# Kernel tuning notes

Measured on AMD Instinct MI355X. Metric: run time of the kernel, lower is better.

The kernel has to match this reference:

```python
import jax, jax.numpy as jnp
import numpy as np

B, S, F, H, C = 8, 512, 32, 256, 128

def _ln(x, g, b, eps=1e-5):
    m = jnp.mean(x, -1, keepdims=True)
    v = jnp.var(x, -1, keepdims=True)
    return (x - m) * jax.lax.rsqrt(v + eps) * g + b

def setup_inputs():
    key = jax.random.key(0)
    ks = jax.random.split(key, 16)
    def n(i, shape, s=0.05):
        return jax.random.normal(ks[i], shape, jnp.float32) * s
    d = {}
    d['x'] = jax.random.normal(ks[0], (B, S, F), jnp.float32)
    d['context'] = jax.random.normal(ks[1], (B, C), jnp.float32)
    # per-feature GRNs, params stacked over F (input_size=1 -> weight is [F,H])
    d['w1'] = n(2, (F, H)); d['b1'] = jnp.zeros((F, H), jnp.float32)
    d['w2'] = n(3, (F, H, H)); d['b2'] = jnp.zeros((F, H), jnp.float32)
    d['wg'] = n(4, (F, H, 2 * H)); d['bg'] = jnp.zeros((F, 2 * H), jnp.float32)
    d['ws'] = n(5, (F, H)); d['bs'] = jnp.zeros((F, H), jnp.float32)
    d['g1'] = jnp.ones((F, H), jnp.float32); d['be1'] = jnp.zeros((F, H), jnp.float32)
    # selection GRN: input F*H, hidden H, output F, context C
    d['sw1'] = n(6, (F * H, H)); d['sb1'] = jnp.zeros((H,), jnp.float32)
    d['sctx'] = n(7, (C, H))
    d['sw2'] = n(8, (H, H)); d['sb2'] = jnp.zeros((H,), jnp.float32)
    d['sgw'] = n(9, (H, 2 * F)); d['sgb'] = jnp.zeros((2 * F,), jnp.float32)
    d['sg'] = jnp.ones((F,), jnp.float32); d['sbt'] = jnp.zeros((F,), jnp.float32)
    d['skw'] = n(10, (F * H, F)); d['skb'] = jnp.zeros((F,), jnp.float32)
    # output GRN: H -> H, identity skip
    d['ow1'] = n(11, (H, H)); d['ob1'] = jnp.zeros((H,), jnp.float32)
    d['ow2'] = n(12, (H, H)); d['ob2'] = jnp.zeros((H,), jnp.float32)
    d['ogw'] = n(13, (H, 2 * H)); d['ogb'] = jnp.zeros((2 * H,), jnp.float32)
    d['og'] = jnp.ones((H,), jnp.float32); d['obt'] = jnp.zeros((H,), jnp.float32)
    return d

def _forward(x, context, w1, b1, w2, b2, wg, bg, ws, bs, g1, be1,
             sw1, sb1, sctx, sw2, sb2, sgw, sgb, sg, sbt, skw, skb,
             ow1, ob1, ow2, ob2, ogw, ogb, og, obt):
    elu = jax.nn.elu
    xe = x[..., None]                                   # [B,S,F,1]
    # --- per-feature GRNs, batched over F (dropout = identity in eval) ---
    h = elu(xe * w1 + b1)                               # [B,S,F,H]
    h = elu(jnp.einsum('bsfh,fhk->bsfk', h, w2) + b2)   # [B,S,F,H]
    gates = jnp.einsum('bsfh,fhk->bsfk', h, wg) + bg    # [B,S,F,2H]
    glu = gates[..., :H] * jax.nn.sigmoid(gates[..., H:])
    skip = xe * ws + bs                                 # skip_layer (1 -> H)
    stacked = _ln(glu + skip, g1, be1)                  # [B,S,F,H]
    # --- selection GRN on flattened features, with context enrichment ---
    flat = stacked.reshape(x.shape[0], x.shape[1], F * H)
    sskip = flat @ skw + skb                            # [B,S,F]
    hs = elu(flat @ sw1 + sb1)
    hs = hs + (context @ sctx)[:, None, :]              # expand ctx over seq
    hs = elu(hs @ sw2 + sb2)
    gg = hs @ sgw + sgb
    glu2 = gg[..., :F] * jax.nn.sigmoid(gg[..., F:])
    weights = jax.nn.softmax(_ln(glu2 + sskip, sg, sbt), axis=-1)  # [B,S,F]
    # --- softmax-weighted feature fusion ---
    combined = jnp.einsum('bsfh,bsf->bsh', stacked, weights)       # [B,S,H]
    # --- output GRN (identity skip) ---
    ho = elu(combined @ ow1 + ob1)
    ho = elu(ho @ ow2 + ob2)
    go = ho @ ogw + ogb
    glu3 = go[..., :H] * jax.nn.sigmoid(go[..., H:])
    out = _ln(glu3 + combined, og, obt)
    return out, weights

def reference(x, context, w1, b1, w2, b2, wg, bg, ws, bs, g1, be1,
              sw1, sb1, sctx, sw2, sb2, sgw, sgb, sg, sbt, skw, skb,
              ow1, ob1, ow2, ob2, ogw, ogb, og, obt):
    return _forward(x, context, w1, b1, w2, b2, wg, bg, ws, bs, g1, be1,
                    sw1, sb1, sctx, sw2, sb2, sgw, sgb, sg, sbt, skw, skb,
                    ow1, ob1, ow2, ob2, ogw, ogb, og, obt)
```

## Files before the change

### kernel.cpp

```cpp
#include <hip/hip_runtime.h>

#define TTOT 4096
#define FDIM 32
#define HDIM 256
#define CDIM 128

__device__ __forceinline__ float eluf(float z){ return z > 0.f ? z : __expf(z) - 1.f; }
__device__ __forceinline__ float sigf(float z){ return 1.f / (1.f + __expf(-z)); }

__device__ __forceinline__ void zero84(float a[8][4]){
#pragma unroll
  for (int t = 0; t < 8; ++t){ a[t][0] = a[t][1] = a[t][2] = a[t][3] = 0.f; }
}

__device__ __forceinline__ void gemm_8x4(const float* __restrict__ A, int lda,
                                         const float* __restrict__ W, int ldw,
                                         int tb, int K, float acc[8][4]){
  for (int h0 = 0; h0 < K; h0 += 8){
    float4 wr[8];
#pragma unroll
    for (int r = 0; r < 8; ++r) wr[r] = *(const float4*)(W + (h0 + r)*ldw);
#pragma unroll
    for (int t = 0; t < 8; ++t){
      const float* ap = A + (tb + t)*lda + h0;
      float4 a0 = *(const float4*)ap;
      float4 a1 = *(const float4*)(ap + 4);
      float av[8] = {a0.x, a0.y, a0.z, a0.w, a1.x, a1.y, a1.z, a1.w};
#pragma unroll
      for (int r = 0; r < 8; ++r){
        acc[t][0] = fmaf(av[r], wr[r].x, acc[t][0]);
        acc[t][1] = fmaf(av[r], wr[r].y, acc[t][1]);
        acc[t][2] = fmaf(av[r], wr[r].z, acc[t][2]);
        acc[t][3] = fmaf(av[r], wr[r].w, acc[t][3]);
      }
    }
  }
}

__device__ __forceinline__ void feature_grn(
    const int f, const int tid, const float* __restrict__ xsf,
    const float* __restrict__ w1, const float* __restrict__ b1,
    const float* __restrict__ w2, const float* __restrict__ b2,
    const float* __restrict__ wg, const float* __restrict__ bg,
    const float* __restrict__ wsk, const float* __restrict__ bsk,
    const float* __restrict__ g1, const float* __restrict__ be1,
    float* __restrict__ bufA, float* __restrict__ bufB,
    float* __restrict__ mS, float* __restrict__ rS)
{
  const int kg = tid & 63, tg = tid >> 6;
  const int k0 = kg*4, tb = tg*8;

  {
    const float w1v = w1[f*HDIM + tid];
    const float b1v = b1[f*HDIM + tid];
#pragma unroll 8
    for (int t = 0; t < 32; ++t) bufA[t*256 + tid] = eluf(xsf[t*8]*w1v + b1v);
  }
  __syncthreads();

  {
    float acc[8][4]; zero84(acc);
    gemm_8x4(bufA, 256, w2 + (size_t)f*65536 + k0, 256, tb, 256, acc);
    const float4 bv = *(const float4*)(b2 + f*HDIM + k0);
#pragma unroll
    for (int t = 0; t < 8; ++t){
      float4 o;
      o.x = eluf(acc[t][0] + bv.x); o.y = eluf(acc[t][1] + bv.y);
      o.z = eluf(acc[t][2] + bv.z); o.w = eluf(acc[t][3] + bv.w);
      *(float4*)(bufB + (tb + t)*256 + k0) = o;
    }
  }
  __syncthreads();

  {
    float accA[8][4], accB[8][4]; zero84(accA); zero84(accB);
    const float* wgf = wg + (size_t)f*131072;
    gemm_8x4(bufB, 256, wgf + k0,       512, tb, 256, accA);
    gemm_8x4(bufB, 256, wgf + 256 + k0, 512, tb, 256, accB);
    const float4 bga = *(const float4*)(bg + f*512 + k0);
    const float4 bgb = *(const float4*)(bg + f*512 + 256 + k0);
    const float4 wsv = *(const float4*)(wsk + f*HDIM + k0);
    const float4 bsv = *(const float4*)(bsk + f*HDIM + k0);
    const float ba[4] = {bga.x, bga.y, bga.z, bga.w};
    const float bb[4] = {bgb.x, bgb.y, bgb.z, bgb.w};
    const float wa[4] = {wsv.x, wsv.y, wsv.z, wsv.w};
    const float sa[4] = {bsv.x, bsv.y, bsv.z, bsv.w};
#pragma unroll
    for (int t = 0; t < 8; ++t){
      const float xv = xsf[(tb + t)*8];
      float o[4];
#pragma unroll
      for (int j = 0; j < 4; ++j){
        const float ga = accA[t][j] + ba[j];
        const float gb = accB[t][j] + bb[j];
        o[j] = ga*sigf(gb) + fmaf(xv, wa[j], sa[j]);
      }
      *(float4*)(bufA + (tb + t)*256 + k0) = make_float4(o[0], o[1], o[2], o[3]);
    }
  }
  __syncthreads();

  {
    const int tt = tid >> 3, j = tid & 7;
    float s = 0.f, s2 = 0.f;
#pragma unroll 8
    for (int i = 0; i < 32; ++i){
      const float v = bufA[tt*256 + j + i*8];
      s += v; s2 = fmaf(v, v, s2);
    }
    s += __shfl_xor(s, 1); s2 += __shfl_xor(s2, 1);
    s += __shfl_xor(s, 2); s2 += __shfl_xor(s2, 2);
    s += __shfl_xor(s, 4); s2 += __shfl_xor(s2, 4);
    if (j == 0){
      const float m = s * (1.f/256.f);
      mS[tt] = m;
      rS[tt] = rsqrtf(s2*(1.f/256.f) - m*m + 1e-5f);
    }
  }
  __syncthreads();

  {
    const float gv = g1[f*HDIM + tid];
    const float bv = be1[f*HDIM + tid];
#pragma unroll 4
    for (int t = 0; t < 32; ++t)
      bufB[t*256 + tid] = (bufA[t*256 + tid] - mS[t])*rS[t]*gv + bv;
  }
  __syncthreads();
}

template<int STORE>
__global__ __launch_bounds__(256, 2) void k_feat(
    const float* __restrict__ x,
    const float* __restrict__ w1, const float* __restrict__ b1,
    const float* __restrict__ w2, const float* __restrict__ b2,
    const float* __restrict__ wg, const float* __restrict__ bg,
    const float* __restrict__ wsk, const float* __restrict__ bsk,
    const float* __restrict__ g1, const float* __restrict__ be1,
    const float* __restrict__ sw1, const float* __restrict__ skw,
    float* __restrict__ z1_part, float* __restrict__ sskip_part,
    float* __restrict__ stacked)
{
  const int t0 = blockIdx.x * 32;
  const int fg = blockIdx.y;
  const int tid = threadIdx.x;
  __shared__ float xs8[32*8];
  __shared__ float mS[32], rS[32];
  __shared__ __align__(16) float bufA[8192];
  __shared__ __align__(16) float bufB[8192];

  {
    const int r = tid >> 3, c = tid & 7;
    xs8[r*8 + c] = x[(t0 + r)*FDIM + fg*8 + c];
  }
  const int kg = tid & 63, tg = tid >> 6;
  const int k0 = kg*4, tb = tg*8;
  const int tt = tid >> 3, j0 = (tid & 7)*4;

  float acc_sel[8][4]; zero84(acc_sel);
  float acc_skip[4] = {0.f, 0.f, 0.f, 0.f};
  __syncthreads();

  for (int i = 0; i < 8; ++i){
    const int f = fg*8 + i;
    feature_grn(f, tid, xs8 + i, w1, b1, w2, b2, wg, bg, wsk, bsk, g1, be1,
                bufA, bufB, mS, rS);
    gemm_8x4(bufB, 256, sw1 + (size_t)f*65536 + k0, 256, tb, 256, acc_sel);
    for (int h = 0; h < 256; h += 4){
      const float4 a = *(const float4*)(bufB + tt*256 + h);
      const size_t rb = ((size_t)f*256 + h)*32 + j0;
      const float4 s0 = *(const float4*)(skw + rb);
      const float4 s1 = *(const float4*)(skw + rb + 32);
      const float4 s2 = *(const float4*)(skw + rb + 64);
      const float4 s3 = *(const float4*)(skw + rb + 96);
      acc_skip[0] = fmaf(a.x, s0.x, fmaf(a.y, s1.x, fmaf(a.z, s2.x, fmaf(a.w, s3.x, acc_skip[0]))));
      acc_skip[1] = fmaf(a.x, s0.y, fmaf(a.y, s1.y, fmaf(a.z, s2.y, fmaf(a.w, s3.y, acc_skip[1]))));
      acc_skip[2] = fmaf(a.x, s0.z, fmaf(a.y, s1.z, fmaf(a.z, s2.z, fmaf(a.w, s3.z, acc_skip[2]))));
      acc_skip[3] = fmaf(a.x, s0.w, fmaf(a.y, s1.w, fmaf(a.z, s2.w, fmaf(a.w, s3.w, acc_skip[3]))));
    }
    if (STORE){
      float* outp = stacked + (size_t)t0*8192 + f*256 + tid;
#pragma unroll 4
      for (int t = 0; t < 32; ++t) outp[(size_t)t*8192] = bufB[t*256 + tid];
    }
  }

  float* zp = z1_part + (size_t)fg*TTOT*HDIM + (size_t)t0*256;
#pragma unroll
  for (int t = 0; t < 8; ++t)
    *(float4*)(zp + (tb + t)*256 + k0) =
        make_float4(acc_sel[t][0], acc_sel[t][1], acc_sel[t][2], acc_sel[t][3]);
  float* sp = sskip_part + (size_t)fg*TTOT*32 + (size_t)t0*32;
  *(float4*)(sp + tt*32 + j0) =
      make_float4(acc_skip[0], acc_skip[1], acc_skip[2], acc_skip[3]);
}

__global__ __launch_bounds__(256, 2) void k_feat2(
    const float* __restrict__ x,
    const float* __restrict__ w1, const float* __restrict__ b1,
    const float* __restrict__ w2, const float* __restrict__ b2,
    const float* __restrict__ wg, const float* __restrict__ bg,
    const float* __restrict__ wsk, const float* __restrict__ bsk,
    const float* __restrict__ g1, const float* __restrict__ be1,
    const float* __restrict__ wts,
    float* __restrict__ cmb_part)
{
  const int t0 = blockIdx.x * 32;
  const int fg = blockIdx.y;
  const int tid = threadIdx.x;
  __shared__ float xs8[32*8];
  __shared__ float wt8[32*8];
  __shared__ float mS[32], rS[32];
  __shared__ __align__(16) float bufA[8192];
  __shared__ __align__(16) float bufB[8192];

  {
    const int r = tid >> 3, c = tid & 7;
    xs8[r*8 + c] = x[(t0 + r)*FDIM + fg*8 + c];
    wt8[r*8 + c] = wts[(t0 + r)*FDIM + fg*8 + c];
  }
  const int kg = tid & 63, tg = tid >> 6;
  const int k0 = kg*4, tb = tg*8;
  float acc_cmb[8][4]; zero84(acc_cmb);
  __syncthreads();

  for (int i = 0; i < 8; ++i){
    const int f = fg*8 + i;
    feature_grn(f, tid, xs8 + i, w1, b1, w2, b2, wg, bg, wsk, bsk, g1, be1,
                bufA, bufB, mS, rS);
#pragma unroll
    for (int t = 0; t < 8; ++t){
      const float wv = wt8[(tb + t)*8 + i];
      const float4 a = *(const float4*)(bufB + (tb + t)*256 + k0);
      acc_cmb[t][0] = fmaf(wv, a.x, acc_cmb[t][0]);
      acc_cmb[t][1] = fmaf(wv, a.y, acc_cmb[t][1]);
      acc_cmb[t][2] = fmaf(wv, a.z, acc_cmb[t][2]);
      acc_cmb[t][3] = fmaf(wv, a.w, acc_cmb[t][3]);
    }
  }
  float* cp = cmb_part + (size_t)fg*TTOT*HDIM + (size_t)t0*256;
#pragma unroll
  for (int t = 0; t < 8; ++t)
    *(float4*)(cp + (tb + t)*256 + k0) =
        make_float4(acc_cmb[t][0], acc_cmb[t][1], acc_cmb[t][2], acc_cmb[t][3]);
}

__global__ __launch_bounds__(256) void k_sel2(
    const float* __restrict__ z1_part,
    const float* __restrict__ sb1,
    const float* __restrict__ context, const float* __restrict__ sctx,
    const float* __restrict__ sw2, const float* __restrict__ sb2,
    const float* __restrict__ sgw, const float* __restrict__ sgb,
    const float* __restrict__ sg, const float* __restrict__ sbt,
    const float* __restrict__ sskip_part, const float* __restrict__ skb,
    float* __restrict__ wout)
{
  const int t0 = blockIdx.x * 32;
  const int tid = threadIdx.x;
  __shared__ __align__(16) float A[8192];
  __shared__ __align__(16) float Bm[8192];
  __shared__ float ggs[32*64];
  __shared__ float pn[32*32];

  float cxv = 0.f;
  {
    const float* cb = context + (size_t)(t0 >> 9)*CDIM;
    for (int c = 0; c < CDIM; ++c) cxv = fmaf(cb[c], sctx[c*HDIM + tid], cxv);
  }
  {
    const float sbv = sb1[tid];
    const float* p0 = z1_part + (size_t)t0*256;
    const float* p1 = p0 + (size_t)TTOT*HDIM;
    const float* p2 = p0 + (size_t)2*TTOT*HDIM;
    const float* p3 = p0 + (size_t)3*TTOT*HDIM;
#pragma unroll 4
    for (int i = 0; i < 32; ++i){
      const int idx = i*256 + tid;
      A[idx] = eluf(p0[idx] + p1[idx] + p2[idx] + p3[idx] + sbv) + cxv;
    }
  }
  __syncthreads();
  const int kg = tid & 63, tg = tid >> 6;
  const int k0 = kg*4, tb = tg*8;
  {
    float acc[8][4]; zero84(acc);
    gemm_8x4(A, 256, sw2 + k0, 256, tb, 256, acc);
    const float4 bv = *(const float4*)(sb2 + k0);
#pragma unroll
    for (int t = 0; t < 8; ++t){
      float4 o;
      o.x = eluf(acc[t][0] + bv.x); o.y = eluf(acc[t][1] + bv.y);
      o.z = eluf(acc[t][2] + bv.z); o.w = eluf(acc[t][3] + bv.w);
      *(float4*)(Bm + (tb + t)*256 + k0) = o;
    }
  }
  __syncthreads();
  {
    const int t = tid >> 3, jg = tid & 7;
    float a8[8] = {0.f,0.f,0.f,0.f,0.f,0.f,0.f,0.f};
    for (int h = 0; h < 256; ++h){
      const float v = Bm[t*256 + h];
      const float4 wA = *(const float4*)(sgw + h*64 + jg*8);
      const float4 wB = *(const float4*)(sgw + h*64 + jg*8 + 4);
      a8[0] = fmaf(v, wA.x, a8[0]); a8[1] = fmaf(v, wA.y, a8[1]);
      a8[2] = fmaf(v, wA.z, a8[2]); a8[3] = fmaf(v, wA.w, a8[3]);
      a8[4] = fmaf(v, wB.x, a8[4]); a8[5] = fmaf(v, wB.y, a8[5]);
      a8[6] = fmaf(v, wB.z, a8[6]); a8[7] = fmaf(v, wB.w, a8[7]);
    }
#pragma unroll
    for (int j = 0; j < 8; ++j) ggs[t*64 + jg*8 + j] = a8[j] + sgb[jg*8 + j];
  }
  __syncthreads();
  for (int i = tid; i < 1024; i += 256){
    const int t = i >> 5, j = i & 31;
    const size_t si = (size_t)(t0 + t)*32 + j;
    const float ss = sskip_part[si] + sskip_part[si + (size_t)TTOT*32]
                   + sskip_part[si + (size_t)2*TTOT*32]
                   + sskip_part[si + (size_t)3*TTOT*32] + skb[j];
    pn[i] = ggs[t*64 + j]*sigf(ggs[t*64 + 32 + j]) + ss;
  }
  __syncthreads();
  {
    const int tt = tid >> 3, j = tid & 7;
    float v[4]; float s = 0.f, s2 = 0.f;
#pragma unroll
    for (int i = 0; i < 4; ++i){ v[i] = pn[tt*32 + j + i*8]; s += v[i]; s2 = fmaf(v[i], v[i], s2); }
    s += __shfl_xor(s, 1); s2 += __shfl_xor(s2, 1);
    s += __shfl_xor(s, 2); s2 += __shfl_xor(s2, 2);
    s += __shfl_xor(s, 4); s2 += __shfl_xor(s2, 4);
    const float m = s*(1.f/32.f);
    const float rstd = rsqrtf(s2*(1.f/32.f) - m*m + 1e-5f);
    float zv[4]; float mx = -1e30f;
#pragma unroll
    for (int i = 0; i < 4; ++i){
      const int fi = j + i*8;
      zv[i] = (v[i] - m)*rstd*sg[fi] + sbt[fi];
      mx = fmaxf(mx, zv[i]);
    }
    mx = fmaxf(mx, __shfl_xor(mx, 1));
    mx = fmaxf(mx, __shfl_xor(mx, 2));
    mx = fmaxf(mx, __shfl_xor(mx, 4));
    float e[4]; float se = 0.f;
#pragma unroll
    for (int i = 0; i < 4; ++i){ e[i] = __expf(zv[i] - mx); se += e[i]; }
    se += __shfl_xor(se, 1);
    se += __shfl_xor(se, 2);
    se += __shfl_xor(se, 4);
    const float inv = 1.f/se;
#pragma unroll
    for (int i = 0; i < 4; ++i) wout[(size_t)(t0 + tt)*32 + j + i*8] = e[i]*inv;
  }
}

__device__ __forceinline__ void output_grn(
    const int tid, const int t0,
    float* __restrict__ cs, float* __restrict__ bufA, float* __restrict__ bufB,
    float* __restrict__ mS, float* __restrict__ rS,
    const float* __restrict__ ow1, const float* __restrict__ ob1,
    const float* __restrict__ ow2, const float* __restrict__ ob2,
    const float* __restrict__ ogw, const float* __restrict__ ogb,
    const float* __restrict__ og, const float* __restrict__ obt,
    float* __restrict__ outp)
{
  const int kg = tid & 63, tg = tid >> 6;
  const int k0 = kg*4, tb = tg*8;
  {
    float acc[8][4]; zero84(acc);
    gemm_8x4(cs, 256, ow1 + k0, 256, tb, 256, acc);
    const float4 bv = *(const float4*)(ob1 + k0);
#pragma unroll
    for (int t = 0; t < 8; ++t){
      float4 o;
      o.x = eluf(acc[t][0] + bv.x); o.y = eluf(acc[t][1] + bv.y);
      o.z = eluf(acc[t][2] + bv.z); o.w = eluf(acc[t][3] + bv.w);
      *(float4*)(bufA + (tb + t)*256 + k0) = o;
    }
  }
  __syncthreads();
  {
    float acc[8][4]; zero84(acc);
    gemm_8x4(bufA, 256, ow2 + k0, 256, tb, 256, acc);
    const float4 bv = *(const float4*)(ob2 + k0);
#pragma unroll
    for (int t = 0; t < 8; ++t){
      float4 o;
      o.x = eluf(acc[t][0] + bv.x); o.y = eluf(acc[t][1] + bv.y);
      o.z = eluf(acc[t][2] + bv.z); o.w = eluf(acc[t][3] + bv.w);
      *(float4*)(bufB + (tb + t)*256 + k0) = o;
    }
  }
  __syncthreads();
  {
    float accA[8][4], accB[8][4]; zero84(accA); zero84(accB);
    gemm_8x4(bufB, 256, ogw + k0,       512, tb, 256, accA);
    gemm_8x4(bufB, 256, ogw + 256 + k0, 512, tb, 256, accB);
    const float4 bga = *(const float4*)(ogb + k0);
    const float4 bgb = *(const float4*)(ogb + 256 + k0);
    const float ba[4] = {bga.x, bga.y, bga.z, bga.w};
    const float bb[4] = {bgb.x, bgb.y, bgb.z, bgb.w};
#pragma unroll
    for (int t = 0; t < 8; ++t){
      const float4 rv = *(const float4*)(cs + (tb + t)*256 + k0);
      const float rr[4] = {rv.x, rv.y, rv.z, rv.w};
      float o[4];
#pragma unroll
      for (int j = 0; j < 4; ++j){
        const float ga = accA[t][j] + ba[j];
        const float gb = accB[t][j] + bb[j];
        o[j] = ga*sigf(gb) + rr[j];
      }
      *(float4*)(bufA + (tb + t)*256 + k0) = make_float4(o[0], o[1], o[2], o[3]);
    }
  }
  __syncthreads();
  {
    const int tt = tid >> 3, j = tid & 7;
    float s = 0.f, s2 = 0.f;
#pragma unroll 8
    for (int i = 0; i < 32; ++i){
      const float v = bufA[tt*256 + j + i*8];
      s += v; s2 = fmaf(v, v, s2);
    }
    s += __shfl_xor(s, 1); s2 += __shfl_xor(s2, 1);
    s += __shfl_xor(s, 2); s2 += __shfl_xor(s2, 2);
    s += __shfl_xor(s, 4); s2 += __shfl_xor(s2, 4);
    if (j == 0){
      const float m = s * (1.f/256.f);
      mS[tt] = m;
      rS[tt] = rsqrtf(s2*(1.f/256.f) - m*m + 1e-5f);
    }
  }
  __syncthreads();
  {
    const float ogv = og[tid], obv = obt[tid];
#pragma unroll 4
    for (int t = 0; t < 32; ++t)
      outp[(size_t)(t0 + t)*256 + tid] = (bufA[t*256 + tid] - mS[t])*rS[t]*ogv + obv;
  }
}

__global__ __launch_bounds__(256) void k_out(
    const float* __restrict__ stacked, const float* __restrict__ wts_in,
    const float* __restrict__ ow1, const float* __restrict__ ob1,
    const float* __restrict__ ow2, const float* __restrict__ ob2,
    const float* __restrict__ ogw, const float* __restrict__ ogb,
    const float* __restrict__ og, const float* __restrict__ obt,
    float* __restrict__ outp)
{
  const int t0 = blockIdx.x * 32;
  const int tid = threadIdx.x;
  __shared__ __align__(16) float cs[8192];
  __shared__ __align__(16) float bufA[8192];
  __shared__ __align__(16) float bufB[8192];
  __shared__ float wts[32*32];
  __shared__ float mS[32], rS[32];
#pragma unroll
  for (int i = 0; i < 4; ++i) wts[tid + i*256] = wts_in[(size_t)t0*32 + tid + i*256];
  __syncthreads();
  for (int t = 0; t < 32; ++t){
    const float* sp = stacked + (size_t)(t0 + t)*8192 + tid;
    float a = 0.f;
#pragma unroll 8
    for (int f2 = 0; f2 < 32; ++f2) a = fmaf(sp[(size_t)f2*256], wts[t*32 + f2], a);
    cs[t*256 + tid] = a;
  }
  __syncthreads();
  output_grn(tid, t0, cs, bufA, bufB, mS, rS, ow1, ob1, ow2, ob2, ogw, ogb, og, obt, outp);
}

__global__ __launch_bounds__(256) void k_out2(
    const float* __restrict__ cmb_part,
    const float* __restrict__ ow1, const float* __restrict__ ob1,
    const float* __restrict__ ow2, const float* __restrict__ ob2,
    const float* __restrict__ ogw, const float* __restrict__ ogb,
    const float* __restrict__ og, const float* __restrict__ obt,
    float* __restrict__ outp)
{
  const int t0 = blockIdx.x * 32;
  const int tid = threadIdx.x;
  __shared__ __align__(16) float cs[8192];
  __shared__ __align__(16) float bufA[8192];
  __shared__ __align__(16) float bufB[8192];
  __shared__ float mS[32], rS[32];
  {
    const float* p0 = cmb_part + (size_t)t0*256;
    const float* p1 = p0 + (size_t)TTOT*HDIM;
    const float* p2 = p0 + (size_t)2*TTOT*HDIM;
    const float* p3 = p0 + (size_t)3*TTOT*HDIM;
#pragma unroll 4
    for (int i = 0; i < 32; ++i){
      const int idx = i*256 + tid;
      cs[idx] = p0[idx] + p1[idx] + p2[idx] + p3[idx];
    }
  }
  __syncthreads();
  output_grn(tid, t0, cs, bufA, bufB, mS, rS, ow1, ob1, ow2, ob2, ogw, ogb, og, obt, outp);
}

extern "C" void kernel_launch(void* const* d_in, const int* in_sizes, int n_in,
                              void* d_out, int out_size, void* d_ws, size_t ws_size,
                              hipStream_t stream){
  (void)in_sizes; (void)n_in; (void)out_size;
  const float* x    = (const float*)d_in[0];
  const float* ctx  = (const float*)d_in[1];
  const float* w1   = (const float*)d_in[2];
  const float* b1   = (const float*)d_in[3];
  const float* w2   = (const float*)d_in[4];
  const float* b2   = (const float*)d_in[5];
  const float* wg   = (const float*)d_in[6];
  const float* bg   = (const float*)d_in[7];
  const float* wsk  = (const float*)d_in[8];
  const float* bsk  = (const float*)d_in[9];
  const float* g1   = (const float*)d_in[10];
  const float* be1  = (const float*)d_in[11];
  const float* sw1  = (const float*)d_in[12];
  const float* sb1  = (const float*)d_in[13];
  const float* sctx = (const float*)d_in[14];
  const float* sw2  = (const float*)d_in[15];
  const float* sb2  = (const float*)d_in[16];
  const float* sgw  = (const float*)d_in[17];
  const float* sgb  = (const float*)d_in[18];
  const float* sg   = (const float*)d_in[19];
  const float* sbt  = (const float*)d_in[20];
  const float* skw  = (const float*)d_in[21];
  const float* skb  = (const float*)d_in[22];
  const float* ow1  = (const float*)d_in[23];
  const float* ob1  = (const float*)d_in[24];
  const float* ow2  = (const float*)d_in[25];
  const float* ob2  = (const float*)d_in[26];
  const float* ogw  = (const float*)d_in[27];
  const float* ogb  = (const float*)d_in[28];
  const float* og   = (const float*)d_in[29];
  const float* obt  = (const float*)d_in[30];

  float* wsf        = (float*)d_ws;
  float* planeBuf   = wsf;
  float* sskip_part = wsf + 4194304;
  float* stacked    = wsf + 4718592;
  const bool fast = ws_size >= (size_t)(4718592 + 33554432)*sizeof(float);

  float* out_main = (float*)d_out;
  float* out_w    = out_main + 1048576;

  if (fast){
    k_feat<1><<<dim3(128, 4), 256, 0, stream>>>(x, w1, b1, w2, b2, wg, bg, wsk, bsk,
                                                g1, be1, sw1, skw, planeBuf, sskip_part, stacked);
    k_sel2<<<128, 256, 0, stream>>>(planeBuf, sb1, ctx, sctx, sw2, sb2, sgw, sgb,
                                    sg, sbt, sskip_part, skb, out_w);
    k_out<<<128, 256, 0, stream>>>(stacked, out_w, ow1, ob1, ow2, ob2, ogw, ogb, og, obt, out_main);
  } else {
    k_feat<0><<<dim3(128, 4), 256, 0, stream>>>(x, w1, b1, w2, b2, wg, bg, wsk, bsk,
                                                g1, be1, sw1, skw, planeBuf, sskip_part, nullptr);
    k_sel2<<<128, 256, 0, stream>>>(planeBuf, sb1, ctx, sctx, sw2, sb2, sgw, sgb,
                                    sg, sbt, sskip_part, skb, out_w);
    k_feat2<<<dim3(128, 4), 256, 0, stream>>>(x, w1, b1, w2, b2, wg, bg, wsk, bsk,
                                              g1, be1, out_w, planeBuf);
    k_out2<<<128, 256, 0, stream>>>(planeBuf, ow1, ob1, ow2, ob2, ogw, ogb, og, obt, out_main);
  }
}
```

Measured before the change: 1.353 ms.

## Pad shared buffers, double-buffer weight loads, and split gate GEMMs to cut registers

After: 2.409 ms. 1.78x slower.

```diff
diff --git a/kernel.cpp b/kernel.cpp
--- a/kernel.cpp
+++ b/kernel.cpp
@@ -4,37 +4,55 @@
 #define FDIM 32
 #define HDIM 256
 #define CDIM 128
+#define LDA  260
+#define LDG  68
+#define LDP  33
 
 __device__ __forceinline__ float eluf(float z){ return z > 0.f ? z : __expf(z) - 1.f; }
 __device__ __forceinline__ float sigf(float z){ return 1.f / (1.f + __expf(-z)); }
 
-__device__ __forceinline__ void zero84(float a[8][4]){
+__device__ __forceinline__ void zero84(float (&a)[8][4]){
 #pragma unroll
   for (int t = 0; t < 8; ++t){ a[t][0] = a[t][1] = a[t][2] = a[t][3] = 0.f; }
+}
+
+__device__ __forceinline__ void fma8(const float* __restrict__ A, int lda, int tb,
+                                     int h0, const float4 (&w)[8], float (&acc)[8][4]){
+#pragma unroll
+  for (int t = 0; t < 8; ++t){
+    const float* ap = A + (tb + t)*lda + h0;
+    float4 a0 = *(const float4*)ap;
+    float4 a1 = *(const float4*)(ap + 4);
+    float av[8] = {a0.x, a0.y, a0.z, a0.w, a1.x, a1.y, a1.z, a1.w};
+#pragma unroll
+    for (int r = 0; r < 8; ++r){
+      acc[t][0] = fmaf(av[r], w[r].x, acc[t][0]);
+      acc[t][1] = fmaf(av[r], w[r].y, acc[t][1]);
+      acc[t][2] = fmaf(av[r], w[r].z, acc[t][2]);
+      acc[t][3] = fmaf(av[r], w[r].w, acc[t][3]);
+    }
+  }
 }
 
 __device__ __forceinline__ void gemm_8x4(const float* __restrict__ A, int lda,
                                          const float* __restrict__ W, int ldw,
-                                         int tb, int K, float acc[8][4]){
-  for (int h0 = 0; h0 < K; h0 += 8){
-    float4 wr[8];
-#pragma unroll
-    for (int r = 0; r < 8; ++r) wr[r] = *(const float4*)(W + (h0 + r)*ldw);
-#pragma unroll
-    for (int t = 0; t < 8; ++t){
-      const float* ap = A + (tb + t)*lda + h0;
-      float4 a0 = *(const float4*)ap;
-      float4 a1 = *(const float4*)(ap + 4);
-      float av[8] = {a0.x, a0.y, a0.z, a0.w, a1.x, a1.y, a1.z, a1.w};
-#pragma unroll
-      for (int r = 0; r < 8; ++r){
-        acc[t][0] = fmaf(av[r], wr[r].x, acc[t][0]);
-        acc[t][1] = fmaf(av[r], wr[r].y, acc[t][1]);
-        acc[t][2] = fmaf(av[r], wr[r].z, acc[t][2]);
-        acc[t][3] = fmaf(av[r], wr[r].w, acc[t][3]);
-      }
-    }
-  }
+                                         int tb, int K, float (&acc)[8][4]){
+  float4 w0[8], w1[8];
+#pragma unroll
+  for (int r = 0; r < 8; ++r) w0[r] = *(const float4*)(W + r*ldw);
+  int h0 = 0;
+  for (; h0 + 16 < K; h0 += 16){
+#pragma unroll
+    for (int r = 0; r < 8; ++r) w1[r] = *(const float4*)(W + (h0 + 8 + r)*ldw);
+    fma8(A, lda, tb, h0, w0, acc);
+#pragma unroll
+    for (int r = 0; r < 8; ++r) w0[r] = *(const float4*)(W + (h0 + 16 + r)*ldw);
+    fma8(A, lda, tb, h0 + 8, w1, acc);
+  }
+#pragma unroll
+  for (int r = 0; r < 8; ++r) w1[r] = *(const float4*)(W + (h0 + 8 + r)*ldw);
+  fma8(A, lda, tb, h0, w0, acc);
+  fma8(A, lda, tb, h0 + 8, w1, acc);
 }
 
 __device__ __forceinline__ void feature_grn(
@@ -54,48 +72,56 @@
     const float w1v = w1[f*HDIM + tid];
     const float b1v = b1[f*HDIM + tid];
 #pragma unroll 8
-    for (int t = 0; t < 32; ++t) bufA[t*256 + tid] = eluf(xsf[t*8]*w1v + b1v);
+    for (int t = 0; t < 32; ++t) bufA[t*LDA + tid] = eluf(xsf[t*8]*w1v + b1v);
   }
   __syncthreads();
 
   {
     float acc[8][4]; zero84(acc);
-    gemm_8x4(bufA, 256, w2 + (size_t)f*65536 + k0, 256, tb, 256, acc);
+    gemm_8x4(bufA, LDA, w2 + (size_t)f*65536 + k0, 256, tb, 256, acc);
     const float4 bv = *(const float4*)(b2 + f*HDIM + k0);
 #pragma unroll
     for (int t = 0; t < 8; ++t){
       float4 o;
       o.x = eluf(acc[t][0] + bv.x); o.y = eluf(acc[t][1] + bv.y);
       o.z = eluf(acc[t][2] + bv.z); o.w = eluf(acc[t][3] + bv.w);
-      *(float4*)(bufB + (tb + t)*256 + k0) = o;
-    }
-  }
-  __syncthreads();
-
-  {
-    float accA[8][4], accB[8][4]; zero84(accA); zero84(accB);
+      *(float4*)(bufB + (tb + t)*LDA + k0) = o;
+    }
+  }
+  __syncthreads();
+
+  {
     const float* wgf = wg + (size_t)f*131072;
-    gemm_8x4(bufB, 256, wgf + k0,       512, tb, 256, accA);
-    gemm_8x4(bufB, 256, wgf + 256 + k0, 512, tb, 256, accB);
-    const float4 bga = *(const float4*)(bg + f*512 + k0);
-    const float4 bgb = *(const float4*)(bg + f*512 + 256 + k0);
-    const float4 wsv = *(const float4*)(wsk + f*HDIM + k0);
-    const float4 bsv = *(const float4*)(bsk + f*HDIM + k0);
-    const float ba[4] = {bga.x, bga.y, bga.z, bga.w};
-    const float bb[4] = {bgb.x, bgb.y, bgb.z, bgb.w};
-    const float wa[4] = {wsv.x, wsv.y, wsv.z, wsv.w};
-    const float sa[4] = {bsv.x, bsv.y, bsv.z, bsv.w};
-#pragma unroll
-    for (int t = 0; t < 8; ++t){
-      const float xv = xsf[(tb + t)*8];
-      float o[4];
-#pragma unroll
-      for (int j = 0; j < 4; ++j){
-        const float ga = accA[t][j] + ba[j];
-        const float gb = accB[t][j] + bb[j];
-        o[j] = ga*sigf(gb) + fmaf(xv, wa[j], sa[j]);
+    {
+      float accA[8][4]; zero84(accA);
+      gemm_8x4(bufB, LDA, wgf + k0, 512, tb, 256, accA);
+      const float4 bga = *(const float4*)(bg + f*512 + k0);
+#pragma unroll
+      for (int t = 0; t < 8; ++t)
+        *(float4*)(bufA + (tb + t)*LDA + k0) =
+            make_float4(accA[t][0] + bga.x, accA[t][1] + bga.y,
+                        accA[t][2] + bga.z, accA[t][3] + bga.w);
+    }
+    {
+      float accB[8][4]; zero84(accB);
+      gemm_8x4(bufB, LDA, wgf + 256 + k0, 512, tb, 256, accB);
+      const float4 bgb = *(const float4*)(bg + f*512 + 256 + k0);
+      const float4 wsv = *(const float4*)(wsk + f*HDIM + k0);
+      const float4 bsv = *(const float4*)(bsk + f*HDIM + k0);
+      const float bb[4] = {bgb.x, bgb.y, bgb.z, bgb.w};
+      const float wa[4] = {wsv.x, wsv.y, wsv.z, wsv.w};
+      const float sa[4] = {bsv.x, bsv.y, bsv.z, bsv.w};
+#pragma unroll
+      for (int t = 0; t < 8; ++t){
+        const float xv = xsf[(tb + t)*8];
+        const float4 gav = *(const float4*)(bufA + (tb + t)*LDA + k0);
+        const float ga[4] = {gav.x, gav.y, gav.z, gav.w};
+        float o[4];
+#pragma unroll
+        for (int j = 0; j < 4; ++j)
+          o[j] = ga[j]*sigf(accB[t][j] + bb[j]) + fmaf(xv, wa[j], sa[j]);
+        *(float4*)(bufA + (tb + t)*LDA + k0) = make_float4(o[0], o[1], o[2], o[3]);
       }
-      *(float4*)(bufA + (tb + t)*256 + k0) = make_float4(o[0], o[1], o[2], o[3]);
     }
   }
   __syncthreads();
@@ -105,7 +131,7 @@
     float s = 0.f, s2 = 0.f;
 #pragma unroll 8
     for (int i = 0; i < 32; ++i){
-      const float v = bufA[tt*256 + j + i*8];
+      const float v = bufA[tt*LDA + j + i*8];
       s += v; s2 = fmaf(v, v, s2);
     }
     s += __shfl_xor(s, 1); s2 += __shfl_xor(s2, 1);
@@ -124,7 +150,7 @@
     const float bv = be1[f*HDIM + tid];
 #pragma unroll 4
     for (int t = 0; t < 32; ++t)
-      bufB[t*256 + tid] = (bufA[t*256 + tid] - mS[t])*rS[t]*gv + bv;
+      bufB[t*LDA + tid] = (bufA[t*LDA + tid] - mS[t])*rS[t]*gv + bv;
   }
   __syncthreads();
 }
@@ -146,8 +172,8 @@
   const int tid = threadIdx.x;
   __shared__ float xs8[32*8];
   __shared__ float mS[32], rS[32];
-  __shared__ __align__(16) float bufA[8192];
-  __shared__ __align__(16) float bufB[8192];
+  __shared__ __align__(16) float bufA[32*LDA];
+  __shared__ __align__(16) float bufB[32*LDA];
 
   {
     const int r = tid >> 3, c = tid & 7;
@@ -165,9 +191,10 @@
     const int f = fg*8 + i;
     feature_grn(f, tid, xs8 + i, w1, b1, w2, b2, wg, bg, wsk, bsk, g1, be1,
                 bufA, bufB, mS, rS);
-    gemm_8x4(bufB, 256, sw1 + (size_t)f*65536 + k0, 256, tb, 256, acc_sel);
+    gemm_8x4(bufB, LDA, sw1 + (size_t)f*65536 + k0, 256, tb, 256, acc_sel);
+#pragma unroll 4
     for (int h = 0; h < 256; h += 4){
-      const float4 a = *(const float4*)(bufB + tt*256 + h);
+      const float4 a = *(const float4*)(bufB + tt*LDA + h);
       const size_t rb = ((size_t)f*256 + h)*32 + j0;
       const float4 s0 = *(const float4*)(skw + rb);
       const float4 s1 = *(const float4*)(skw + rb + 32);
@@ -181,7 +208,7 @@
     if (STORE){
       float* outp = stacked + (size_t)t0*8192 + f*256 + tid;
 #pragma unroll 4
-      for (int t = 0; t < 32; ++t) outp[(size_t)t*8192] = bufB[t*256 + tid];
+      for (int t = 0; t < 32; ++t) outp[(size_t)t*8192] = bufB[t*LDA + tid];
     }
   }
 
@@ -211,8 +238,8 @@
   __shared__ float xs8[32*8];
   __shared__ float wt8[32*8];
   __shared__ float mS[32], rS[32];
-  __shared__ __align__(16) float bufA[8192];
-  __shared__ __align__(16) float bufB[8192];
+  __shared__ __align__(16) float bufA[32*LDA];
+  __shared__ __align__(16) float bufB[32*LDA];
 
   {
     const int r = tid >> 3, c = tid & 7;
@@ -231,7 +258,7 @@
 #pragma unroll
     for (int t = 0; t < 8; ++t){
       const float wv = wt8[(tb + t)*8 + i];
-      const float4 a = *(const float4*)(bufB + (tb + t)*256 + k0);
+      const float4 a = *(const float4*)(bufB + (tb + t)*LDA + k0);
       acc_cmb[t][0] = fmaf(wv, a.x, acc_cmb[t][0]);
       acc_cmb[t][1] = fmaf(wv, a.y, acc_cmb[t][1]);
       acc_cmb[t][2] = fmaf(wv, a.z, acc_cmb[t][2]);
@@ -257,14 +284,15 @@
 {
   const int t0 = blockIdx.x * 32;
   const int tid = threadIdx.x;
-  __shared__ __align__(16) float A[8192];
-  __shared__ __align__(16) float Bm[8192];
-  __shared__ float ggs[32*64];
-  __shared__ float pn[32*32];
+  __shared__ __align__(16) float A[32*LDA];
+  __shared__ __align__(16) float Bm[32*LDA];
+  __shared__ float ggs[32*LDG];
+  __shared__ float pn[32*LDP];
 
   float cxv = 0.f;
   {
     const float* cb = context + (size_t)(t0 >> 9)*CDIM;
+#pragma unroll 8
     for (int c = 0; c < CDIM; ++c) cxv = fmaf(cb[c], sctx[c*HDIM + tid], cxv);
   }
   {
@@ -275,8 +303,8 @@
     const float* p3 = p0 + (size_t)3*TTOT*HDIM;
 #pragma unroll 4
     for (int i = 0; i < 32; ++i){
-      const int idx = i*256 + tid;
-      A[idx] = eluf(p0[idx] + p1[idx] + p2[idx] + p3[idx] + sbv) + cxv;
+      const int gi = i*256 + tid;
+      A[i*LDA + tid] = eluf(p0[gi] + p1[gi] + p2[gi] + p3[gi] + sbv) + cxv;
     }
   }
   __syncthreads();
@@ -284,22 +312,23 @@
   const int k0 = kg*4, tb = tg*8;
   {
     float acc[8][4]; zero84(acc);
-    gemm_8x4(A, 256, sw2 + k0, 256, tb, 256, acc);
+    gemm_8x4(A, LDA, sw2 + k0, 256, tb, 256, acc);
     const float4 bv = *(const float4*)(sb2 + k0);
 #pragma unroll
     for (int t = 0; t < 8; ++t){
       float4 o;
       o.x = eluf(acc[t][0] + bv.x); o.y = eluf(acc[t][1] + bv.y);
       o.z = eluf(acc[t][2] + bv.z); o.w = eluf(acc[t][3] + bv.w);
-      *(float4*)(Bm + (tb + t)*256 + k0) = o;
+      *(float4*)(Bm + (tb + t)*LDA + k0) = o;
     }
   }
   __syncthreads();
   {
     const int t = tid >> 3, jg = tid & 7;
     float a8[8] = {0.f,0.f,0.f,0.f,0.f,0.f,0.f,0.f};
+#pragma unroll 4
     for (int h = 0; h < 256; ++h){
-      const float v = Bm[t*256 + h];
+      const float v = Bm[t*LDA + h];
       const float4 wA = *(const float4*)(sgw + h*64 + jg*8);
       const float4 wB = *(const float4*)(sgw + h*64 + jg*8 + 4);
       a8[0] = fmaf(v, wA.x, a8[0]); a8[1] = fmaf(v, wA.y, a8[1]);
@@ -308,7 +337,7 @@
       a8[6] = fmaf(v, wB.z, a8[6]); a8[7] = fmaf(v, wB.w, a8[7]);
     }
 #pragma unroll
-    for (int j = 0; j < 8; ++j) ggs[t*64 + jg*8 + j] = a8[j] + sgb[jg*8 + j];
+    for (int j = 0; j < 8; ++j) ggs[t*LDG + jg*8 + j] = a8[j] + sgb[jg*8 + j];
   }
   __syncthreads();
   for (int i = tid; i < 1024; i += 256){
@@ -317,14 +346,14 @@
     const float ss = sskip_part[si] + sskip_part[si + (size_t)TTOT*32]
                    + sskip_part[si + (size_t)2*TTOT*32]
                    + sskip_part[si + (size_t)3*TTOT*32] + skb[j];
-    pn[i] = ggs[t*64 + j]*sigf(ggs[t*64 + 32 + j]) + ss;
+    pn[t*LDP + j] = ggs[t*LDG + j]*sigf(ggs[t*LDG + 32 + j]) + ss;
   }
   __syncthreads();
   {
     const int tt = tid >> 3, j = tid & 7;
     float v[4]; float s = 0.f, s2 = 0.f;
 #pragma unroll
-    for (int i = 0; i < 4; ++i){ v[i] = pn[tt*32 + j + i*8]; s += v[i]; s2 = fmaf(v[i], v[i], s2); }
+    for (int i = 0; i < 4; ++i){ v[i] = pn[tt*LDP + j + i*8]; s += v[i]; s2 = fmaf(v[i], v[i], s2); }
     s += __shfl_xor(s, 1); s2 += __shfl_xor(s2, 1);
     s += __shfl_xor(s, 2); s2 += __shfl_xor(s2, 2);
     s += __shfl_xor(s, 4); s2 += __shfl_xor(s2, 4);
@@ -366,50 +395,59 @@
   const int k0 = kg*4, tb = tg*8;
   {
     float acc[8][4]; zero84(acc);
-    gemm_8x4(cs, 256, ow1 + k0, 256, tb, 256, acc);
+    gemm_8x4(cs, LDA, ow1 + k0, 256, tb, 256, acc);
     const float4 bv = *(const float4*)(ob1 + k0);
 #pragma unroll
     for (int t = 0; t < 8; ++t){
       float4 o;
       o.x = eluf(acc[t][0] + bv.x); o.y = eluf(acc[t][1] + bv.y);
       o.z = eluf(acc[t][2] + bv.z); o.w = eluf(acc[t][3] + bv.w);
-      *(float4*)(bufA + (tb + t)*256 + k0) = o;
+      *(float4*)(bufA + (tb + t)*LDA + k0) = o;
     }
   }
   __syncthreads();
   {
     float acc[8][4]; zero84(acc);
-    gemm_8x4(bufA, 256, ow2 + k0, 256, tb, 256, acc);
+    gemm_8x4(bufA, LDA, ow2 + k0, 256, tb, 256, acc);
     const float4 bv = *(const float4*)(ob2 + k0);
 #pragma unroll
     for (int t = 0; t < 8; ++t){
       float4 o;
       o.x = eluf(acc[t][0] + bv.x); o.y = eluf(acc[t][1] + bv.y);
       o.z = eluf(acc[t][2] + bv.z); o.w = eluf(acc[t][3] + bv.w);
-      *(float4*)(bufB + (tb + t)*256 + k0) = o;
-    }
-  }
-  __syncthreads();
-  {
-    float accA[8][4], accB[8][4]; zero84(accA); zero84(accB);
-    gemm_8x4(bufB, 256, ogw + k0,       512, tb, 256, accA);
-    gemm_8x4(bufB, 256, ogw + 256 + k0, 512, tb, 256, accB);
-    const float4 bga = *(const float4*)(ogb + k0);
-    const float4 bgb = *(const float4*)(ogb + 256 + k0);
-    const float ba[4] = {bga.x, bga.y, bga.z, bga.w};
-    const float bb[4] = {bgb.x, bgb.y, bgb.z, bgb.w};
-#pragma unroll
-    for (int t = 0; t < 8; ++t){
-      const float4 rv = *(const float4*)(cs + (tb + t)*256 + k0);
-      const float rr[4] = {rv.x, rv.y, rv.z, rv.w};
-      float o[4];
-#pragma unroll
-      for (int j = 0; j < 4; ++j){
-        const float ga = accA[t][j] + ba[j];
-        const float gb = accB[t][j] + bb[j];
-        o[j] = ga*sigf(gb) + rr[j];
+      *(float4*)(bufB + (tb + t)*LDA + k0) = o;
+    }
+  }
+  __syncthreads();
+  {
+    const float* wgf = ogw;
+    {
+      float accA[8][4]; zero84(accA);
+      gemm_8x4(bufB, LDA, wgf + k0, 512, tb, 256, accA);
+      const float4 bga = *(const float4*)(ogb + k0);
+#pragma unroll
+      for (int t = 0; t < 8; ++t)
+        *(float4*)(bufA + (tb + t)*LDA + k0) =
+            make_float4(accA[t][0] + bga.x, accA[t][1] + bga.y,
+                        accA[t][2] + bga.z, accA[t][3] + bga.w);
+    }
+    {
+      float accB[8][4]; zero84(accB);
+      gemm_8x4(bufB, LDA, wgf + 256 + k0, 512, tb, 256, accB);
+      const float4 bgb = *(const float4*)(ogb + 256 + k0);
+      const float bb[4] = {bgb.x, bgb.y, bgb.z, bgb.w};
+#pragma unroll
+      for (int t = 0; t < 8; ++t){
+        const float4 rv = *(const float4*)(cs + (tb + t)*LDA + k0);
+        const float rr[4] = {rv.x, rv.y, rv.z, rv.w};
+        const float4 gav = *(const float4*)(bufA + (tb + t)*LDA + k0);
+        const float ga[4] = {gav.x, gav.y, gav.z, gav.w};
+        float o[4];
+#pragma unroll
+        for (int j = 0; j < 4; ++j)
+          o[j] = ga[j]*sigf(accB[t][j] + bb[j]) + rr[j];
+        *(float4*)(bufA + (tb + t)*LDA + k0) = make_float4(o[0], o[1], o[2], o[3]);
       }
-      *(float4*)(bufA + (tb + t)*256 + k0) = make_float4(o[0], o[1], o[2], o[3]);
     }
   }
   __syncthreads();
@@ -418,7 +456,7 @@
     float s = 0.f, s2 = 0.f;
 #pragma unroll 8
     for (int i = 0; i < 32; ++i){
-      const float v = bufA[tt*256 + j + i*8];
+      const float v = bufA[tt*LDA + j + i*8];
       s += v; s2 = fmaf(v, v, s2);
     }
     s += __shfl_xor(s, 1); s2 += __shfl_xor(s2, 1);
@@ -435,7 +473,7 @@
     const float ogv = og[tid], obv = obt[tid];
 #pragma unroll 4
     for (int t = 0; t < 32; ++t)
-      outp[(size_t)(t0 + t)*256 + tid] = (bufA[t*256 + tid] - mS[t])*rS[t]*ogv + obv;
+      outp[(size_t)(t0 + t)*256 + tid] = (bufA[t*LDA + tid] - mS[t])*rS[t]*ogv + obv;
   }
 }
 
@@ -449,9 +487,9 @@
 {
   const int t0 = blockIdx.x * 32;
   const int tid = threadIdx.x;
-  __shared__ __align__(16) float cs[8192];
-  __shared__ __align__(16) float bufA[8192];
-  __shared__ __align__(16) float bufB[8192];
+  __shared__ __align__(16) float cs[32*LDA];
+  __shared__ __align__(16) float bufA[32*LDA];
+  __shared__ __align__(16) float bufB[32*LDA];
   __shared__ float wts[32*32];
   __shared__ float mS[32], rS[32];
 #pragma unroll
@@ -462,7 +500,7 @@
     float a = 0.f;
 #pragma unroll 8
     for (int f2 = 0; f2 < 32; ++f2) a = fmaf(sp[(size_t)f2*256], wts[t*32 + f2], a);
-    cs[t*256 + tid] = a;
+    cs[t*LDA + tid] = a;
   }
   __syncthreads();
   output_grn(tid, t0, cs, bufA, bufB, mS, rS, ow1, ob1, ow2, ob2, ogw, ogb, og, obt, outp);
@@ -478,9 +516,9 @@
 {
   const int t0 = blockIdx.x * 32;
   const int tid = threadIdx.x;
-  __shared__ __align__(16) float cs[8192];
-  __shared__ __align__(16) float bufA[8192];
-  __shared__ __align__(16) float bufB[8192];
+  __shared__ __align__(16) float cs[32*LDA];
+  __shared__ __align__(16) float bufA[32*LDA];
+  __shared__ __align__(16) float bufB[32*LDA];
   __shared__ float mS[32], rS[32];
   {
     const float* p0 = cmb_part + (size_t)t0*256;
@@ -489,8 +527,8 @@
     const float* p3 = p0 + (size_t)3*TTOT*HDIM;
 #pragma unroll 4
     for (int i = 0; i < 32; ++i){
-      const int idx = i*256 + tid;
-      cs[idx] = p0[idx] + p1[idx] + p2[idx] + p3[idx];
+      const int gi = i*256 + tid;
+      cs[i*LDA + tid] = p0[gi] + p1[gi] + p2[gi] + p3[gi];
     }
   }
   __syncthreads();
```
